# Kernel tuning notes

Hardware: AMD Instinct MI355X
Metric: run time of the kernel (lower is better)

The kernel has to match this reference:

```python
import jax, jax.numpy as jnp
import numpy as np

L, D, H, FF, I, MAXREL = 6, 512, 8, 2048, 50, 128
HD = D // H
NREL = 2 * MAXREL + 1
EPS = 1e-5


def setup_inputs() -> dict:
    key = jax.random.key(0)
    ks = jax.random.split(key, 32)
    s = 0.02
    p = {
        'x': jax.random.normal(ks[0], (16, 512, I), dtype=jnp.float32),
        'in_w': jax.random.normal(ks[1], (I, D)) * s,
        'in_b': jnp.zeros((D,), jnp.float32),
        'Wq': jax.random.normal(ks[2], (L, D, D)) * s,
        'Wk': jax.random.normal(ks[3], (L, D, D)) * s,
        'Wv': jax.random.normal(ks[4], (L, D, D)) * s,
        'Wo': jax.random.normal(ks[5], (L, D, D)) * s,
        'bo': jnp.zeros((L, D), jnp.float32),
        'rel_emb': jax.random.normal(ks[6], (L, NREL, HD)) * s,
        'w1': jax.random.normal(ks[7], (L, D, FF)) * s,
        'b1': jnp.zeros((L, FF), jnp.float32),
        'w2': jax.random.normal(ks[8], (L, FF, D)) * s,
        'b2': jnp.zeros((L, D), jnp.float32),
        'ln1_g': jnp.ones((L, D), jnp.float32),
        'ln1_b': jnp.zeros((L, D), jnp.float32),
        'ln2_g': jnp.ones((L, D), jnp.float32),
        'ln2_b': jnp.zeros((L, D), jnp.float32),
        'on_g': jnp.ones((D,), jnp.float32),
        'on_b': jnp.zeros((D,), jnp.float32),
        'p1_w': jax.random.normal(ks[9], (D, D // 2)) * s,
        'p1_b': jnp.zeros((D // 2,), jnp.float32),
        'p2_w': jax.random.normal(ks[10], (D // 2, 1)) * s,
        'p2_b': jnp.zeros((1,), jnp.float32),
    }
    return p


def _layer_norm(x, g, b):
    m = jnp.mean(x, axis=-1, keepdims=True)
    v = jnp.mean(jnp.square(x - m), axis=-1, keepdims=True)
    return (x - m) * jax.lax.rsqrt(v + EPS) * g + b


def _sinusoidal_pe(seq_len, d_model):
    pos = jnp.arange(seq_len, dtype=jnp.float32)[:, None]
    div = jnp.exp(jnp.arange(0, d_model, 2, dtype=jnp.float32) * (-jnp.log(10000.0) / d_model))
    pe = jnp.zeros((seq_len, d_model), jnp.float32)
    pe = pe.at[:, 0::2].set(jnp.sin(pos * div))
    pe = pe.at[:, 1::2].set(jnp.cos(pos * div))
    return pe


def reference(x, in_w, in_b, Wq, Wk, Wv, Wo, bo, rel_emb, w1, b1, w2, b2,
              ln1_g, ln1_b, ln2_g, ln2_b, on_g, on_b, p1_w, p1_b, p2_w, p2_b):
    B, S, _ = x.shape
    scale = jnp.sqrt(jnp.float32(HD))
    # relative position index matrix [S, S] in [0, 2*MAXREL]
    r = jnp.arange(S)
    rel_idx = jnp.clip(r[None, :] - r[:, None], -MAXREL, MAXREL) + MAXREL

    h = x @ in_w + in_b                       # [B,S,D]
    h = h + _sinusoidal_pe(S, D)

    for l in range(L):
        q = (h @ Wq[l]).reshape(B, S, H, HD).transpose(0, 2, 1, 3)  # [B,H,S,hd]
        k = (h @ Wk[l]).reshape(B, S, H, HD).transpose(0, 2, 1, 3)
        v = (h @ Wv[l]).reshape(B, S, H, HD).transpose(0, 2, 1, 3)
        scores = jnp.einsum('bhqd,bhkd->bhqk', q, k) / scale
        rel = rel_emb[l][rel_idx]             # [S,S,hd]
        scores = scores + jnp.einsum('bhqd,qkd->bhqk', q, rel)  # rel bias is NOT scaled (matches source)
        attn = jax.nn.softmax(scores, axis=-1)
        ctx = jnp.einsum('bhqk,bhkd->bhqd', attn, v)
        ctx = ctx.transpose(0, 2, 1, 3).reshape(B, S, D)
        attn_out = ctx @ Wo[l] + bo[l]
        h = _layer_norm(h + attn_out, ln1_g[l], ln1_b[l])
        ff = jax.nn.relu(h @ w1[l] + b1[l]) @ w2[l] + b2[l]
        h = _layer_norm(h + ff, ln2_g[l], ln2_b[l])

    h = _layer_norm(h, on_g, on_b)
    out = jax.nn.relu(h @ p1_w + p1_b) @ p2_w + p2_b  # [B,S,1]
    return out
```

## Files before the change

kernel.cpp:

```cpp
#include <hip/hip_runtime.h>

typedef unsigned short u16;
typedef unsigned int   u32;
typedef short   short8  __attribute__((ext_vector_type(8)));
typedef float   floatx4 __attribute__((ext_vector_type(4)));
typedef int     intx4   __attribute__((ext_vector_type(4)));

#define NTOK 8192
#define SEQ  512
#define NLAYER 6

#define OFF_WT   ((size_t)0)
#define OFF_HB   ((size_t)38010880)
#define OFF_QKV  ((size_t)46399488)
#define OFF_CTX  ((size_t)71565312)
#define OFF_GOUT ((size_t)79953920)
#define OFF_FF   ((size_t)96731136)
#define OFF_HD1  ((size_t)130285568)
#define OFF_VT   OFF_FF
#define OFF_RELB OFF_HD1

#define LSTRIDE 3145728
#define P1T_OFF 18874368

__device__ __forceinline__ float b2f(u16 v) { return __uint_as_float(((u32)v) << 16); }
__device__ __forceinline__ float lo16(u32 v) { return __uint_as_float(v << 16); }
__device__ __forceinline__ float hi16(u32 v) { return __uint_as_float(v & 0xffff0000u); }
__device__ __forceinline__ u16 f2b(float f) {
  u32 x = __float_as_uint(f);
  return (u16)((x + 0x7fffu + ((x >> 16) & 1u)) >> 16);
}
__device__ __forceinline__ u32 pack2(float a, float b) {
  return (u32)f2b(a) | ((u32)f2b(b) << 16);
}
__device__ __forceinline__ u32 cvtpk(float a, float b) {
  u32 r;
  asm("v_cvt_pk_bf16_f32 %0, %1, %2" : "=v"(r) : "v"(a), "v"(b));
  return r;
}

typedef __attribute__((address_space(1))) void* gas_t;
typedef __attribute__((address_space(3))) void* las_t;

__global__ __launch_bounds__(256) void transpose_all(
    const float* __restrict__ Wq, const float* __restrict__ Wk,
    const float* __restrict__ Wv, const float* __restrict__ Wo,
    const float* __restrict__ w1, const float* __restrict__ w2,
    const float* __restrict__ p1, u16* __restrict__ wT)
{
  __shared__ u16 tile[64][65];
  const int tb = blockIdx.x;
  const float* src; u16* dst; int R, C, tidx;
  if (tb < 4608) {
    const int l = tb / 768, r = tb % 768;
    const size_t lofs = (size_t)l * LSTRIDE;
    if (r < 256) {
      const int m = r >> 6; tidx = r & 63; R = 512; C = 512;
      const float* bases[4] = {Wq, Wk, Wv, Wo};
      src = bases[m] + (size_t)l * 262144;
      dst = wT + lofs + (size_t)m * 262144;
    } else if (r < 512) {
      tidx = r - 256; R = 512; C = 2048;
      src = w1 + (size_t)l * 1048576; dst = wT + lofs + 1048576;
    } else {
      tidx = r - 512; R = 2048; C = 512;
      src = w2 + (size_t)l * 1048576; dst = wT + lofs + 2097152;
    }
  } else {
    tidx = tb - 4608; R = 512; C = 256;
    src = p1; dst = wT + P1T_OFF;
  }
  const int tcn = C >> 6;
  const int tr = tidx / tcn, tc = tidx % tcn;
  const int th = threadIdx.x;
  {
    const int lr = th >> 2, cg = (th & 3) * 16;
    const float* sp = src + (size_t)(tr*64 + lr) * C + tc*64 + cg;
    float4 f0 = *(const float4*)(sp);
    float4 f1 = *(const float4*)(sp + 4);
    float4 f2 = *(const float4*)(sp + 8);
    float4 f3 = *(const float4*)(sp + 12);
    u16* tp = &tile[lr][cg];
    tp[0]=f2b(f0.x); tp[1]=f2b(f0.y); tp[2]=f2b(f0.z); tp[3]=f2b(f0.w);
    tp[4]=f2b(f1.x); tp[5]=f2b(f1.y); tp[6]=f2b(f1.z); tp[7]=f2b(f1.w);
    tp[8]=f2b(f2.x); tp[9]=f2b(f2.y); tp[10]=f2b(f2.z); tp[11]=f2b(f2.w);
    tp[12]=f2b(f3.x); tp[13]=f2b(f3.y); tp[14]=f2b(f3.z); tp[15]=f2b(f3.w);
  }
  __syncthreads();
  {
    const int oc = th >> 2, rg = (th & 3) * 16;
    u32 wds[8];
    #pragma unroll
    for (int i = 0; i < 8; ++i)
      wds[i] = (u32)tile[rg + 2*i][oc] | ((u32)tile[rg + 2*i + 1][oc] << 16);
    const int n  = tc*64 + oc;
    const int k0 = tr*64 + rg;
    const int nb = n >> 7, j = (n >> 4) & 7, lr = n & 15;
    const int kc = k0 >> 5, lq = (k0 >> 3) & 3;
    const int KC = R >> 5;
    u16* base = dst + (((((size_t)nb*KC + kc) << 3) + j) << 9);
    uint4 o0; o0.x=wds[0]; o0.y=wds[1]; o0.z=wds[2]; o0.w=wds[3];
    uint4 o1; o1.x=wds[4]; o1.y=wds[5]; o1.z=wds[6]; o1.w=wds[7];
    *(uint4*)(base + (lq*16 + lr)*8)       = o0;
    *(uint4*)(base + ((lq+1)*16 + lr)*8)   = o1;
  }
}

__global__ __launch_bounds__(128) void input_proj(
    const float* __restrict__ x, const float* __restrict__ w, const float* __restrict__ ib,
    u16* __restrict__ hb)
{
  const int row = blockIdx.x, t = threadIdx.x;
  const int s = row & (SEQ - 1);
  __shared__ float xs[50];
  if (t < 50) xs[t] = x[row*50 + t];
  __syncthreads();
  const int d0 = t * 4;
  float4 acc = *(const float4*)(ib + d0);
  #pragma unroll
  for (int i = 0; i < 50; ++i) {
    const float4 wv = *(const float4*)(w + i*512 + d0);
    const float xv = xs[i];
    acc.x = fmaf(xv, wv.x, acc.x);
    acc.y = fmaf(xv, wv.y, acc.y);
    acc.z = fmaf(xv, wv.z, acc.z);
    acc.w = fmaf(xv, wv.w, acc.w);
  }
  const float cexp = -0.017988946f;
  const float dv0 = __expf((float)d0 * cexp);
  const float dv1 = __expf((float)(d0 + 2) * cexp);
  float s0, c0, s1, c1;
  __sincosf((float)s * dv0, &s0, &c0);
  __sincosf((float)s * dv1, &s1, &c1);
  acc.x += s0; acc.y += c0; acc.z += s1; acc.w += c1;
  u32* hp = (u32*)(hb + (size_t)row*512 + d0);
  hp[0] = pack2(acc.x, acc.y);
  hp[1] = pack2(acc.z, acc.w);
}

__global__ __launch_bounds__(256, 4) void gemm_bt(
    const u16* __restrict__ A, const u16* __restrict__ Bt,
    const float* __restrict__ bias,
    float* __restrict__ outF0, float* __restrict__ outF1, u16* __restrict__ outB,
    u16* __restrict__ vTout,
    const int M, const int N, const int K, const int kLen, const int flags)
{
  __shared__ __align__(16) u16 As[2][8192];
  const int id = blockIdx.x;
  const int xcd = id & 7, rest = id >> 3;
  const int bm = (rest & 7) * 8 + xcd;
  const int bn = rest >> 3;
  const int z = blockIdx.y;
  const int kOff = z * kLen;
  const int m0 = bm << 7, n0 = bn << 7;
  const int tid = threadIdx.x;
  const int wave = tid >> 6, lane = tid & 63;
  const int wr = (wave >> 1) << 6, wc = (wave & 1) << 6;
  const int lrow = lane & 15, lquad = lane >> 4;

  floatx4 acc[4][4];
  #pragma unroll
  for (int i = 0; i < 4; ++i)
    #pragma unroll
    for (int j = 0; j < 4; ++j) { floatx4 zz = {0.f,0.f,0.f,0.f}; acc[i][j] = zz; }

  const u16* a0p = A + (size_t)m0 * K + kOff;
  const int c0 = tid, c1 = 256 + tid;
  const int ar0 = c0 >> 2, as0 = (c0 & 3) * 8;
  const int ar1 = c1 >> 2, as1 = (c1 & 3) * 8;
  const int KC = K >> 5;
  const u16* bW = Bt + ((((size_t)bn*KC + (kOff >> 5)) * 8 + (wave & 1) * 4) << 9) + lane*8;

#define STAGE_A(buf, k0) do {                                                                  \
    __builtin_amdgcn_global_load_lds((gas_t)(a0p + (size_t)ar0*K + (k0) + as0),                \
                                     (las_t)(&As[buf][c0*8]), 16, 0, 0);                       \
    __builtin_amdgcn_global_load_lds((gas_t)(a0p + (size_t)ar1*K + (k0) + as1),                \
                                     (las_t)(&As[buf][c1*8]), 16, 0, 0);                       \
    __builtin_amdgcn_global_load_lds((gas_t)(a0p + (size_t)ar0*K + (k0) + 32 + as0),           \
                                     (las_t)(&As[buf][4096 + c0*8]), 16, 0, 0);                \
    __builtin_amdgcn_global_load_lds((gas_t)(a0p + (size_t)ar1*K + (k0) + 32 + as1),           \
                                     (las_t)(&As[buf][4096 + c1*8]), 16, 0, 0);                \
  } while (0)

  const int nst = kLen >> 6;
  STAGE_A(0, 0);
  __syncthreads();

  int cur = 0;
  for (int t = 0; t < nst; ++t) {
    const u16* bc = bW + (size_t)(2*t) * 4096;
    short8 b0[4], b1[4];
    #pragma unroll
    for (int j = 0; j < 4; ++j) b0[j] = *(const short8*)(bc + j*512);
    if (t + 1 < nst) STAGE_A(cur ^ 1, (t + 1) * 64);
    #pragma unroll
    for (int j = 0; j < 4; ++j) b1[j] = *(const short8*)(bc + 4096 + j*512);
    {
      short8 af[4];
      #pragma unroll
      for (int i = 0; i < 4; ++i) af[i] = *(const short8*)&As[cur][(wr + i*16 + lrow)*32 + lquad*8];
      #pragma unroll
      for (int i = 0; i < 4; ++i)
        #pragma unroll
        for (int j = 0; j < 4; ++j)
          acc[i][j] = __builtin_amdgcn_mfma_f32_16x16x32_bf16(b0[j], af[i], acc[i][j], 0, 0, 0);
    }
    {
      short8 af[4];
      #pragma unroll
      for (int i = 0; i < 4; ++i) af[i] = *(const short8*)&As[cur][4096 + (wr + i*16 + lrow)*32 + lquad*8];
      #pragma unroll
      for (int i = 0; i < 4; ++i)
        #pragma unroll
        for (int j = 0; j < 4; ++j)
          acc[i][j] = __builtin_amdgcn_mfma_f32_16x16x32_bf16(b1[j], af[i], acc[i][j], 0, 0, 0);
    }
    if (t + 1 < nst) { __syncthreads(); cur ^= 1; }
  }
#undef STAGE_A

  if ((flags & 4) && n0 >= 1024) {
    #pragma unroll
    for (int i = 0; i < 4; ++i) {
      const int row = m0 + wr + i*16 + lrow;
      const int bb = row >> 9, s = row & 511;
      #pragma unroll
      for (int j = 0; j < 4; ++j) {
        const int cm0 = (n0 - 1024) + wc + j*16 + lquad*4;
        #pragma unroll
        for (int v = 0; v < 4; ++v) {
          const int cm = cm0 + v;
          const int hh = cm >> 6, d = cm & 63;
          vTout[((size_t)(bb*8 + hh)*64 + d)*512 + s] = f2b(acc[i][j][v]);
        }
      }
    }
    return;
  }

  float* outF = (z == 0) ? outF0 : outF1;
  const bool hasb = ((flags & 1) != 0) && (z == 0);
  const bool dorelu = (flags & 2) != 0;
  #pragma unroll
  for (int i = 0; i < 4; ++i) {
    const int row = m0 + wr + i*16 + lrow;
    #pragma unroll
    for (int j = 0; j < 4; ++j) {
      const int colbase = n0 + wc + j*16 + lquad*4;
      float4 bv4 = make_float4(0.f, 0.f, 0.f, 0.f);
      if (hasb) bv4 = *(const float4*)(bias + colbase);
      float v0 = acc[i][j][0] + bv4.x;
      float v1 = acc[i][j][1] + bv4.y;
      float v2 = acc[i][j][2] + bv4.z;
      float v3 = acc[i][j][3] + bv4.w;
      if (dorelu) {
        v0 = fmaxf(v0, 0.f); v1 = fmaxf(v1, 0.f);
        v2 = fmaxf(v2, 0.f); v3 = fmaxf(v3, 0.f);
      }
      const size_t off = (size_t)row * N + colbase;
      if (outB) {
        uint2 o; o.x = pack2(v0, v1); o.y = pack2(v2, v3);
        *(uint2*)(outB + off) = o;
      } else {
        *(float4*)(outF + off) = make_float4(v0, v1, v2, v3);
      }
    }
  }
}

__global__ __launch_bounds__(256) void cvt_rel_all(
    const float* __restrict__ rel, u16* __restrict__ relB)
{
  const int i = blockIdx.x*256 + threadIdx.x;
  if (i < 6*257*64) {
    const int l = i / 16448, rem = i % 16448;
    relB[l*17408 + rem] = f2b(rel[i]);
  }
}

__global__ __launch_bounds__(256, 3) void attn_mfma(
    const u16* __restrict__ qkv, const u16* __restrict__ vT,
    const u16* __restrict__ relB, u16* __restrict__ ctx)
{
  const int id = blockIdx.x;
  const int xcd = id & 7, g = (id >> 3) & 15, qt = id >> 7;
  const int bh = xcd*16 + g;
  const int b = bh >> 3, h = bh & 7;
  const int t = threadIdx.x, w = t >> 6, lane = t & 63;
  const int lr = lane & 15, quad = lane >> 4;

  __shared__ __align__(16) u16 Ks[64*72];
  __shared__ __align__(16) u16 Vs[64*72];
  __shared__ __align__(16) u16 Pr[64*274];

  const size_t token0 = (size_t)b*512 + qt*64;
  const int srow = t >> 2, scol = (t & 3) * 16;
  const u16* kbase = qkv + (size_t)b*512*1536 + 512 + h*64;
  const u16* vbase = vT + (size_t)bh*64*512;

  short8 af0, af1;
  {
    const u16* qp = qkv + (token0 + w*16 + lr)*1536 + h*64 + quad*8;
    af0 = *(const short8*)(qp);
    af1 = *(const short8*)(qp + 32);
  }

  uint4 kr0, kr1, vr0, vr1;
  {
    const u16* kp = kbase + (size_t)srow*1536 + scol;
    kr0 = *(const uint4*)kp; kr1 = *(const uint4*)(kp + 8);
    const u16* vp = vbase + (size_t)srow*512 + scol;
    vr0 = *(const uint4*)vp; vr1 = *(const uint4*)(vp + 8);
  }

  #pragma unroll 4
  for (int nt = 0; nt < 17; ++nt) {
    const u16* rp = relB + (nt*16 + lr)*64 + quad*8;
    short8 rb0 = *(const short8*)(rp);
    short8 rb1 = *(const short8*)(rp + 32);
    floatx4 c = {0.f,0.f,0.f,0.f};
    c = __builtin_amdgcn_mfma_f32_16x16x32_bf16(af0, rb0, c, 0, 0, 0);
    c = __builtin_amdgcn_mfma_f32_16x16x32_bf16(af1, rb1, c, 0, 0, 0);
    #pragma unroll
    for (int r = 0; r < 4; ++r)
      Pr[(w*16 + quad*4 + r)*274 + nt*16 + lr] = f2b(c[r] * 1.44269504f);
  }

  floatx4 oacc[4];
  float lacc = 0.f;
  #pragma unroll
  for (int n = 0; n < 4; ++n) { floatx4 zz = {0.f,0.f,0.f,0.f}; oacc[n] = zz; }

  const int qglob = qt*64 + w*16 + lr;
  const int prbase = (w*16 + lr)*274 + 128;

  const float prLo = b2f(Pr[prbase - 128]);
  const float prHi = b2f(Pr[prbase + 128]);

  for (int kt = 0; kt < 8; ++kt) {
    __syncthreads();
    *(uint4*)&Ks[srow*72 + scol]     = kr0;
    *(uint4*)&Ks[srow*72 + scol + 8] = kr1;
    *(uint4*)&Vs[srow*72 + scol]     = vr0;
    *(uint4*)&Vs[srow*72 + scol + 8] = vr1;
    __syncthreads();

    if (kt < 7) {
      const u16* kp = kbase + (size_t)((kt+1)*64 + srow)*1536 + scol;
      kr0 = *(const uint4*)kp; kr1 = *(const uint4*)(kp + 8);
      const u16* vp = vbase + (size_t)srow*512 + (kt+1)*64 + scol;
      vr0 = *(const uint4*)vp; vr1 = *(const uint4*)(vp + 8);
    }

    floatx4 s4[4];
    __builtin_amdgcn_s_setprio(1);
    #pragma unroll
    for (int nt = 0; nt < 4; ++nt) {
      short8 kb0 = *(const short8*)&Ks[(nt*16 + lr)*72 + quad*8];
      short8 kb1 = *(const short8*)&Ks[(nt*16 + lr)*72 + 32 + quad*8];
      floatx4 c = {0.f,0.f,0.f,0.f};
      c = __builtin_amdgcn_mfma_f32_16x16x32_bf16(kb0, af0, c, 0, 0, 0);
      c = __builtin_amdgcn_mfma_f32_16x16x32_bf16(kb1, af1, c, 0, 0, 0);
      s4[nt] = c;
    }
    __builtin_amdgcn_s_setprio(0);

    const int tmin = kt*64 - (qt*64 + w*16 + 15);
    const int tmax = tmin + 78;
    u32 wq[4][2];
    const int kq = kt*64 + quad*4 - qglob;
    if (tmin >= 128 || tmax <= -128) {
      const float pc = (tmin >= 128) ? prHi : prLo;
      #pragma unroll
      for (int nt = 0; nt < 4; ++nt) {
        float p[4];
        #pragma unroll
        for (int r = 0; r < 4; ++r)
          p[r] = exp2f(fmaf(s4[nt][r], 0.18033688f, pc));
        lacc += (p[0] + p[1]) + (p[2] + p[3]);
        wq[nt][0] = cvtpk(p[0], p[1]);
        wq[nt][1] = cvtpk(p[2], p[3]);
      }
    } else if (tmin >= -128 && tmax <= 128) {
      #pragma unroll
      for (int nt = 0; nt < 4; ++nt) {
        const int dbase = kq + nt*16;
        float p[4];
        #pragma unroll
        for (int r = 0; r < 4; ++r)
          p[r] = exp2f(fmaf(s4[nt][r], 0.18033688f, b2f(Pr[prbase + dbase + r])));
        lacc += (p[0] + p[1]) + (p[2] + p[3]);
        wq[nt][0] = cvtpk(p[0], p[1]);
        wq[nt][1] = cvtpk(p[2], p[3]);
      }
    } else {
      #pragma unroll
      for (int nt = 0; nt < 4; ++nt) {
        const int dbase = kq + nt*16;
        float p[4];
        #pragma unroll
        for (int r = 0; r < 4; ++r) {
          int dd = dbase + r;
          dd = dd < -128 ? -128 : (dd > 128 ? 128 : dd);
          p[r] = exp2f(fmaf(s4[nt][r], 0.18033688f, b2f(Pr[prbase + dd])));
        }
        lacc += (p[0] + p[1]) + (p[2] + p[3]);
        wq[nt][0] = cvtpk(p[0], p[1]);
        wq[nt][1] = cvtpk(p[2], p[3]);
      }
    }

    intx4 pw0; pw0.x = (int)wq[0][0]; pw0.y = (int)wq[0][1];
               pw0.z = (int)wq[1][0]; pw0.w = (int)wq[1][1];
    intx4 pw1; pw1.x = (int)wq[2][0]; pw1.y = (int)wq[2][1];
               pw1.z = (int)wq[3][0]; pw1.w = (int)wq[3][1];
    const short8 pf0 = __builtin_bit_cast(short8, pw0);
    const short8 pf1 = __builtin_bit_cast(short8, pw1);

    __builtin_amdgcn_s_setprio(1);
    #pragma unroll
    for (int nd = 0; nd < 4; ++nd) {
      const int vrow = (nd*16 + lr)*72;
      uint2 a0 = *(const uint2*)&Vs[vrow + quad*4];
      uint2 a1 = *(const uint2*)&Vs[vrow + 16 + quad*4];
      uint2 a2 = *(const uint2*)&Vs[vrow + 32 + quad*4];
      uint2 a3 = *(const uint2*)&Vs[vrow + 48 + quad*4];
      intx4 v0; v0.x = (int)a0.x; v0.y = (int)a0.y; v0.z = (int)a1.x; v0.w = (int)a1.y;
      intx4 v1; v1.x = (int)a2.x; v1.y = (int)a2.y; v1.z = (int)a3.x; v1.w = (int)a3.y;
      const short8 vb0 = __builtin_bit_cast(short8, v0);
      const short8 vb1 = __builtin_bit_cast(short8, v1);
      oacc[nd] = __builtin_amdgcn_mfma_f32_16x16x32_bf16(vb0, pf0, oacc[nd], 0, 0, 0);
      oacc[nd] = __builtin_amdgcn_mfma_f32_16x16x32_bf16(vb1, pf1, oacc[nd], 0, 0, 0);
    }
    __builtin_amdgcn_s_setprio(0);
  }

  lacc += __shfl_xor(lacc, 16);
  lacc += __shfl_xor(lacc, 32);

  {
    const float inv = 1.f / lacc;
    u16* cp = ctx + (token0 + w*16 + lr)*512 + h*64;
    #pragma unroll
    for (int nd = 0; nd < 4; ++nd) {
      const int d = nd*16 + quad*4;
      uint2 o;
      o.x = pack2(oacc[nd][0]*inv, oacc[nd][1]*inv);
      o.y = pack2(oacc[nd][2]*inv, oacc[nd][3]*inv);
      *(uint2*)(cp + d) = o;
    }
  }
}

__global__ __launch_bounds__(128) void ln_kernel(
    const u16* __restrict__ resB, const float* __restrict__ add0,
    const float* __restrict__ add1,
    const float* __restrict__ g, const float* __restrict__ be,
    u16* __restrict__ hb)
{
  const int row = blockIdx.x, t = threadIdx.x;
  const size_t base = (size_t)row * 512;
  const u32 r0 = *(const u32*)(resB + base + t*4);
  const u32 r1 = *(const u32*)(resB + base + t*4 + 2);
  float x0 = lo16(r0), x1 = hi16(r0), x2 = lo16(r1), x3 = hi16(r1);
  if (add0) {
    const float4 a = *(const float4*)(add0 + base + t*4);
    x0 += a.x; x1 += a.y; x2 += a.z; x3 += a.w;
  }
  if (add1) {
    const float4 a = *(const float4*)(add1 + base + t*4);
    x0 += a.x; x1 += a.y; x2 += a.z; x3 += a.w;
  }
  float s = x0 + x1 + x2 + x3;
  #pragma unroll
  for (int off = 32; off > 0; off >>= 1) s += __shfl_down(s, off);
  __shared__ float red[2];
  const int wv = t >> 6, ln = t & 63;
  if (ln == 0) red[wv] = s;
  __syncthreads();
  const float mean = (red[0] + red[1]) * (1.f/512.f);
  const float dx0 = x0-mean, dx1 = x1-mean, dx2 = x2-mean, dx3 = x3-mean;
  float vs = dx0*dx0 + dx1*dx1 + dx2*dx2 + dx3*dx3;
  __syncthreads();
  #pragma unroll
  for (int off = 32; off > 0; off >>= 1) vs += __shfl_down(vs, off);
  if (ln == 0) red[wv] = vs;
  __syncthreads();
  const float var = (red[0] + red[1]) * (1.f/512.f);
  const float inv = 1.f / sqrtf(var + 1e-5f);
  const float4 gv = *(const float4*)(g + t*4);
  const float4 bv = *(const float4*)(be + t*4);
  const float y0 = dx0*inv*gv.x + bv.x;
  const float y1 = dx1*inv*gv.y + bv.y;
  const float y2 = dx2*inv*gv.z + bv.z;
  const float y3 = dx3*inv*gv.w + bv.w;
  u32* hp = (u32*)(hb + base + t*4);
  hp[0] = pack2(y0, y1); hp[1] = pack2(y2, y3);
}

__global__ __launch_bounds__(256) void head2_kernel(
    const u16* __restrict__ hd1, const float* __restrict__ p2w,
    const float* __restrict__ p2b, float* __restrict__ out)
{
  const int wv = threadIdx.x >> 6, ln = threadIdx.x & 63;
  const int row = blockIdx.x * 4 + wv;
  const u16* hp = hd1 + (size_t)row * 256 + ln*4;
  const u32 h0 = *(const u32*)hp, h1 = *(const u32*)(hp + 2);
  const float4 w = *(const float4*)(p2w + ln*4);
  float acc = lo16(h0)*w.x + hi16(h0)*w.y + lo16(h1)*w.z + hi16(h1)*w.w;
  #pragma unroll
  for (int off = 1; off < 64; off <<= 1) acc += __shfl_xor(acc, off);
  if (ln == 0) out[row] = acc + p2b[0];
}

extern "C" void kernel_launch(void* const* d_in, const int* in_sizes, int n_in,
                              void* d_out, int out_size, void* d_ws, size_t ws_size,
                              hipStream_t stream) {
  (void)in_sizes; (void)n_in; (void)out_size; (void)ws_size;
  const float* X    = (const float*)d_in[0];
  const float* INW  = (const float*)d_in[1];
  const float* INB  = (const float*)d_in[2];
  const float* WQ   = (const float*)d_in[3];
  const float* WK   = (const float*)d_in[4];
  const float* WV   = (const float*)d_in[5];
  const float* WO   = (const float*)d_in[6];
  const float* BO   = (const float*)d_in[7];
  const float* REL  = (const float*)d_in[8];
  const float* W1   = (const float*)d_in[9];
  const float* B1   = (const float*)d_in[10];
  const float* W2   = (const float*)d_in[11];
  const float* B2   = (const float*)d_in[12];
  const float* LN1G = (const float*)d_in[13];
  const float* LN1B = (const float*)d_in[14];
  const float* LN2G = (const float*)d_in[15];
  const float* LN2B = (const float*)d_in[16];
  const float* ONG  = (const float*)d_in[17];
  const float* ONB  = (const float*)d_in[18];
  const float* P1W  = (const float*)d_in[19];
  const float* P1B  = (const float*)d_in[20];
  const float* P2W  = (const float*)d_in[21];
  const float* P2B  = (const float*)d_in[22];
  float* out = (float*)d_out;

  char* ws = (char*)d_ws;
  u16*   wT    = (u16*)(ws + OFF_WT);
  u16*   hB    = (u16*)(ws + OFF_HB);
  u16*   qkv   = (u16*)(ws + OFF_QKV);
  u16*   ctx   = (u16*)(ws + OFF_CTX);
  float* gout0 = (float*)(ws + OFF_GOUT);
  float* gout1 = (float*)(ws + OFF_QKV);
  u16*   ff    = (u16*)(ws + OFF_FF);
  u16*   hd1   = (u16*)(ws + OFF_HD1);
  u16*   vTb   = (u16*)(ws + OFF_VT);
  u16*   relBa = (u16*)(ws + OFF_RELB);

  transpose_all<<<4640, 256, 0, stream>>>(WQ, WK, WV, WO, W1, W2, P1W, wT);
  cvt_rel_all<<<386, 256, 0, stream>>>(REL, relBa);
  input_proj<<<NTOK, 128, 0, stream>>>(X, INW, INB, hB);

  for (int l = 0; l < NLAYER; ++l) {
    const u16* wTl = wT + (size_t)l * LSTRIDE;
    gemm_bt<<<dim3(768,1), 256, 0, stream>>>(hB, wTl, nullptr, nullptr, nullptr, qkv, vTb,
                                             8192, 1536, 512, 512, 4);
    attn_mfma<<<1024, 256, 0, stream>>>(qkv, vTb, relBa + l*17408, ctx);
    gemm_bt<<<dim3(256,2), 256, 0, stream>>>(ctx, wTl + 786432, BO + l*512,
                                             gout0, gout1, nullptr, nullptr,
                                             8192, 512, 512, 256, 1);
    ln_kernel<<<NTOK, 128, 0, stream>>>(hB, gout0, gout1, LN1G + l*512, LN1B + l*512, hB);
    gemm_bt<<<dim3(1024,1), 256, 0, stream>>>(hB, wTl + 1048576, B1 + l*2048,
                                              nullptr, nullptr, ff, nullptr,
                                              8192, 2048, 512, 512, 3);
    gemm_bt<<<dim3(256,2), 256, 0, stream>>>(ff, wTl + 2097152, B2 + l*512,
                                             gout0, gout1, nullptr, nullptr,
                                             8192, 512, 2048, 1024, 1);
    ln_kernel<<<NTOK, 128, 0, stream>>>(hB, gout0, gout1, LN2G + l*512, LN2B + l*512, hB);
  }
  ln_kernel<<<NTOK, 128, 0, stream>>>(hB, nullptr, nullptr, ONG, ONB, hB);
  gemm_bt<<<dim3(128,1), 256, 0, stream>>>(hB, wT + P1T_OFF, P1B,
                                           nullptr, nullptr, hd1, nullptr,
                                           8192, 256, 512, 512, 3);
  head2_kernel<<<2048, 256, 0, stream>>>(hd1, P2W, P2B, out);
}
```

Baseline: 1.096 ms.

## Shrink attention LDS: load V directly from global, XOR-swizzle K tile, raise occupancy

The attention kernel drops the V shared-memory tile and has each lane read its V MFMA fragments straight from global memory every key tile. The K tile loses its padding and uses an XOR swizzle to avoid bank conflicts. The relative-bias table shrinks to 256 columns, with the last column stored separately. Together these cut LDS use so launch bounds can ask for 4 blocks per CU instead of 3. The trade-off is uncoalesced 8-byte global V loads inside the loop, no prefetch of V, and more register pressure.

```diff
diff --git a/kernel.cpp b/kernel.cpp
--- a/kernel.cpp
+++ b/kernel.cpp
@@ -278,7 +278,7 @@
   }
 }
 
-__global__ __launch_bounds__(256, 3) void attn_mfma(
+__global__ __launch_bounds__(256, 4) void attn_mfma(
     const u16* __restrict__ qkv, const u16* __restrict__ vT,
     const u16* __restrict__ relB, u16* __restrict__ ctx)
 {
@@ -289,9 +289,8 @@
   const int t = threadIdx.x, w = t >> 6, lane = t & 63;
   const int lr = lane & 15, quad = lane >> 4;
 
-  __shared__ __align__(16) u16 Ks[64*72];
-  __shared__ __align__(16) u16 Vs[64*72];
-  __shared__ __align__(16) u16 Pr[64*274];
+  __shared__ __align__(16) u16 Ks[64*64];
+  __shared__ __align__(16) u16 Pr[64*256];
 
   const size_t token0 = (size_t)b*512 + qt*64;
   const int srow = t >> 2, scol = (t & 3) * 16;
@@ -305,16 +304,14 @@
     af1 = *(const short8*)(qp + 32);
   }
 
-  uint4 kr0, kr1, vr0, vr1;
+  uint4 kr0, kr1;
   {
     const u16* kp = kbase + (size_t)srow*1536 + scol;
     kr0 = *(const uint4*)kp; kr1 = *(const uint4*)(kp + 8);
-    const u16* vp = vbase + (size_t)srow*512 + scol;
-    vr0 = *(const uint4*)vp; vr1 = *(const uint4*)(vp + 8);
   }
 
   #pragma unroll 4
-  for (int nt = 0; nt < 17; ++nt) {
+  for (int nt = 0; nt < 16; ++nt) {
     const u16* rp = relB + (nt*16 + lr)*64 + quad*8;
     short8 rb0 = *(const short8*)(rp);
     short8 rb1 = *(const short8*)(rp + 32);
@@ -323,8 +320,23 @@
     c = __builtin_amdgcn_mfma_f32_16x16x32_bf16(af1, rb1, c, 0, 0, 0);
     #pragma unroll
     for (int r = 0; r < 4; ++r)
-      Pr[(w*16 + quad*4 + r)*274 + nt*16 + lr] = f2b(c[r] * 1.44269504f);
-  }
+      Pr[(w*16 + quad*4 + r)*256 + nt*16 + lr] = f2b(c[r] * 1.44269504f);
+  }
+  {
+    const u16* rp = relB + (256 + lr)*64 + quad*8;
+    short8 rb0 = *(const short8*)(rp);
+    short8 rb1 = *(const short8*)(rp + 32);
+    floatx4 c = {0.f,0.f,0.f,0.f};
+    c = __builtin_amdgcn_mfma_f32_16x16x32_bf16(af0, rb0, c, 0, 0, 0);
+    c = __builtin_amdgcn_mfma_f32_16x16x32_bf16(af1, rb1, c, 0, 0, 0);
+    if (lr == 0) {
+      #pragma unroll
+      for (int r = 0; r < 4; ++r)
+        Ks[w*16 + quad*4 + r] = f2b(c[r] * 1.44269504f);
+    }
+  }
+  const float prHi = b2f(Ks[w*16 + lr]);
+  const float prLo = b2f(Pr[(w*16 + lr)*256]);
 
   floatx4 oacc[4];
   float lacc = 0.f;
@@ -332,32 +344,41 @@
   for (int n = 0; n < 4; ++n) { floatx4 zz = {0.f,0.f,0.f,0.f}; oacc[n] = zz; }
 
   const int qglob = qt*64 + w*16 + lr;
-  const int prbase = (w*16 + lr)*274 + 128;
-
-  const float prLo = b2f(Pr[prbase - 128]);
-  const float prHi = b2f(Pr[prbase + 128]);
+  const int prbase = (w*16 + lr)*256 + 128;
 
   for (int kt = 0; kt < 8; ++kt) {
     __syncthreads();
-    *(uint4*)&Ks[srow*72 + scol]     = kr0;
-    *(uint4*)&Ks[srow*72 + scol + 8] = kr1;
-    *(uint4*)&Vs[srow*72 + scol]     = vr0;
-    *(uint4*)&Vs[srow*72 + scol + 8] = vr1;
+    {
+      const int swz = (srow & 7) << 4;
+      char* kb = (char*)Ks;
+      *(uint4*)(kb + ((srow*128 + scol*2) ^ swz))      = kr0;
+      *(uint4*)(kb + ((srow*128 + scol*2 + 16) ^ swz)) = kr1;
+    }
     __syncthreads();
 
+    uint2 va[4][4];
+    #pragma unroll
+    for (int nd = 0; nd < 4; ++nd) {
+      const u16* vp = vbase + (size_t)(nd*16 + lr)*512 + kt*64 + quad*4;
+      va[nd][0] = *(const uint2*)(vp);
+      va[nd][1] = *(const uint2*)(vp + 16);
+      va[nd][2] = *(const uint2*)(vp + 32);
+      va[nd][3] = *(const uint2*)(vp + 48);
+    }
     if (kt < 7) {
       const u16* kp = kbase + (size_t)((kt+1)*64 + srow)*1536 + scol;
       kr0 = *(const uint4*)kp; kr1 = *(const uint4*)(kp + 8);
-      const u16* vp = vbase + (size_t)srow*512 + (kt+1)*64 + scol;
-      vr0 = *(const uint4*)vp; vr1 = *(const uint4*)(vp + 8);
     }
 
     floatx4 s4[4];
     __builtin_amdgcn_s_setprio(1);
     #pragma unroll
     for (int nt = 0; nt < 4; ++nt) {
-      short8 kb0 = *(const short8*)&Ks[(nt*16 + lr)*72 + quad*8];
-      short8 kb1 = *(const short8*)&Ks[(nt*16 + lr)*72 + 32 + quad*8];
+      const int row = nt*16 + lr;
+      const char* kbp = (const char*)Ks + row*128;
+      const int swz = (lr & 7) << 4;
+      short8 kb0 = *(const short8*)(kbp + ((quad*16) ^ swz));
+      short8 kb1 = *(const short8*)(kbp + ((64 + quad*16) ^ swz));
       floatx4 c = {0.f,0.f,0.f,0.f};
       c = __builtin_amdgcn_mfma_f32_16x16x32_bf16(kb0, af0, c, 0, 0, 0);
       c = __builtin_amdgcn_mfma_f32_16x16x32_bf16(kb1, af1, c, 0, 0, 0);
@@ -381,7 +402,7 @@
         wq[nt][0] = cvtpk(p[0], p[1]);
         wq[nt][1] = cvtpk(p[2], p[3]);
       }
-    } else if (tmin >= -128 && tmax <= 128) {
+    } else if (tmin >= -128 && tmax <= 127) {
       #pragma unroll
       for (int nt = 0; nt < 4; ++nt) {
         const int dbase = kq + nt*16;
@@ -400,9 +421,10 @@
         float p[4];
         #pragma unroll
         for (int r = 0; r < 4; ++r) {
-          int dd = dbase + r;
-          dd = dd < -128 ? -128 : (dd > 128 ? 128 : dd);
-          p[r] = exp2f(fmaf(s4[nt][r], 0.18033688f, b2f(Pr[prbase + dd])));
+          const int dd = dbase + r;
+          int di = dd < -128 ? -128 : (dd > 127 ? 127 : dd);
+          const float bias = (dd >= 128) ? prHi : b2f(Pr[prbase + di]);
+          p[r] = exp2f(fmaf(s4[nt][r], 0.18033688f, bias));
         }
         lacc += (p[0] + p[1]) + (p[2] + p[3]);
         wq[nt][0] = cvtpk(p[0], p[1]);
@@ -420,13 +442,10 @@
     __builtin_amdgcn_s_setprio(1);
     #pragma unroll
     for (int nd = 0; nd < 4; ++nd) {
-      const int vrow = (nd*16 + lr)*72;
-      uint2 a0 = *(const uint2*)&Vs[vrow + quad*4];
-      uint2 a1 = *(const uint2*)&Vs[vrow + 16 + quad*4];
-      uint2 a2 = *(const uint2*)&Vs[vrow + 32 + quad*4];
-      uint2 a3 = *(const uint2*)&Vs[vrow + 48 + quad*4];
-      intx4 v0; v0.x = (int)a0.x; v0.y = (int)a0.y; v0.z = (int)a1.x; v0.w = (int)a1.y;
-      intx4 v1; v1.x = (int)a2.x; v1.y = (int)a2.y; v1.z = (int)a3.x; v1.w = (int)a3.y;
+      intx4 v0; v0.x = (int)va[nd][0].x; v0.y = (int)va[nd][0].y;
+                v0.z = (int)va[nd][1].x; v0.w = (int)va[nd][1].y;
+      intx4 v1; v1.x = (int)va[nd][2].x; v1.y = (int)va[nd][2].y;
+                v1.z = (int)va[nd][3].x; v1.w = (int)va[nd][3].y;
       const short8 vb0 = __builtin_bit_cast(short8, v0);
       const short8 vb1 = __builtin_bit_cast(short8, v1);
       oacc[nd] = __builtin_amdgcn_mfma_f32_16x16x32_bf16(vb0, pf0, oacc[nd], 0, 0, 0);
```

Result: slower. 1.359 ms (+24.0%).
